# Performance work log

Hardware: AMD Instinct MI355X
Metric: run time of the kernel (lower is better)

Reference implementation:

```python
import jax, jax.numpy as jnp
import numpy as np
from jax import lax

FEAT_STRIDE = 16
N_ANCHOR = 9
PRE_NMS = 3000
POST_NMS = 300
NMS_THRESH = 0.7
MIN_SIZE = 16.0
SCALE = 1.0


def anchor_template():
    # base_size=16, ratios x scales, ratio-major flattening (matches torch loop order)
    base = 16.0
    ratios = jnp.array([0.5, 1.0, 2.0], jnp.float32)
    scales = jnp.array([8.0, 16.0, 32.0], jnp.float32)
    h = (base * scales[None, :] * jnp.sqrt(ratios)[:, None]).reshape(-1)   # [9]
    w = (base * scales[None, :] * jnp.sqrt(1.0 / ratios)[:, None]).reshape(-1)
    cy = cx = base / 2.0
    return jnp.stack([cy - h / 2, cx - w / 2, cy + h / 2, cx + w / 2], axis=1)  # [9,4] (y1,x1,y2,x2)


def shifted_anchors(hh, ww):
    base = anchor_template()
    sy = jnp.arange(hh, dtype=jnp.float32) * FEAT_STRIDE
    sx = jnp.arange(ww, dtype=jnp.float32) * FEAT_STRIDE
    sxg, syg = jnp.meshgrid(sx, sy)  # 'xy' indexing -> [hh,ww], row-major h,w ravel
    shift = jnp.stack([syg.ravel(), sxg.ravel(), syg.ravel(), sxg.ravel()], axis=1)  # [K,4]
    return (shift[:, None, :] + base[None, :, :]).reshape(-1, 4)  # [K*9,4]


def loc2bbox(anchors, loc):
    ah = anchors[:, 2] - anchors[:, 0]
    aw = anchors[:, 3] - anchors[:, 1]
    acy = anchors[:, 0] + 0.5 * ah
    acx = anchors[:, 1] + 0.5 * aw
    dy, dx, dh, dw = loc[:, 0], loc[:, 1], loc[:, 2], loc[:, 3]
    cy = dy * ah + acy
    cx = dx * aw + acx
    h = jnp.exp(dh) * ah
    w = jnp.exp(dw) * aw
    return jnp.stack([cy - 0.5 * h, cx - 0.5 * w, cy + 0.5 * h, cx + 0.5 * w], axis=1)


def pairwise_iou(b):
    area = (b[:, 2] - b[:, 0]) * (b[:, 3] - b[:, 1])  # [P]
    y1 = jnp.maximum(b[:, None, 0], b[None, :, 0])
    x1 = jnp.maximum(b[:, None, 1], b[None, :, 1])
    y2 = jnp.minimum(b[:, None, 2], b[None, :, 2])
    x2 = jnp.minimum(b[:, None, 3], b[None, :, 3])
    inter = jnp.clip(y2 - y1, 0.0) * jnp.clip(x2 - x1, 0.0)
    union = area[:, None] + area[None, :] - inter
    return jnp.where(union > 0.0, inter / union, 0.0)


def conv2d(x, W, b, pad):
    y = lax.conv_general_dilated(x, W, (1, 1), ((pad, pad), (pad, pad)),
                                 dimension_numbers=('NCHW', 'OIHW', 'NCHW'))
    return y + b[None, :, None, None]


def propose_one(loc, score, anchors, img_h, img_w):
    # loc [A,4], score [A] (fg prob)
    boxes = loc2bbox(anchors, loc)
    boxes = jnp.stack([jnp.clip(boxes[:, 0], 0.0, img_h),
                       jnp.clip(boxes[:, 1], 0.0, img_w),
                       jnp.clip(boxes[:, 2], 0.0, img_h),
                       jnp.clip(boxes[:, 3], 0.0, img_w)], axis=1)
    min_sz = MIN_SIZE * SCALE
    valid = ((boxes[:, 2] - boxes[:, 0]) >= min_sz) & ((boxes[:, 3] - boxes[:, 1]) >= min_sz)
    s = jnp.where(valid, score, -jnp.inf)
    top_s, idx = lax.top_k(s, PRE_NMS)           # sorted descending
    b = boxes[idx]                               # [PRE_NMS,4]
    iou = pairwise_iou(b)                        # [PRE_NMS,PRE_NMS]

    def body(i, keep):
        suppressed = jnp.any(keep & (iou[:, i] > NMS_THRESH))
        return keep.at[i].set(~suppressed)

    keep = lax.fori_loop(0, PRE_NMS, body, jnp.zeros(PRE_NMS, bool))
    keep = keep & jnp.isfinite(top_s)
    rank = jnp.where(keep, jnp.arange(PRE_NMS), PRE_NMS)
    order = jnp.argsort(rank)[:POST_NMS]
    roi_valid = keep[order]
    rois = jnp.where(roi_valid[:, None], b[order], 0.0)
    return rois, roi_valid


def reference(x, W1, b1, Ws, bs, Wl, bl, img_h, img_w):
    n, _, hh, ww = x.shape
    anchors = shifted_anchors(hh, ww)                       # [hh*ww*9, 4]
    h = jax.nn.relu(conv2d(x, W1, b1, 1))                   # [n,512,hh,ww]
    rpn_locs = conv2d(h, Wl, bl, 0).transpose(0, 2, 3, 1).reshape(n, -1, 4)
    rpn_scores_raw = conv2d(h, Ws, bs, 0).transpose(0, 2, 3, 1)  # [n,hh,ww,18]
    sc = rpn_scores_raw.reshape(n, hh, ww, N_ANCHOR, 2)
    fg = jax.nn.softmax(sc, axis=-1)[..., 1].reshape(n, -1)      # [n,A]
    rpn_scores = rpn_scores_raw.reshape(n, -1, 2)
    rois, roi_valid = jax.vmap(lambda l, s: propose_one(l, s, anchors, float(img_h), float(img_w)))(rpn_locs, fg)
    return rpn_locs, rpn_scores, rois, roi_valid, anchors


def setup_inputs() -> dict:
    key = jax.random.key(0)
    ks = jax.random.split(key, 4)
    n, c, hh, ww = 4, 512, 64, 64
    x = jax.random.normal(ks[0], (n, c, hh, ww), jnp.float32)
    W1 = jax.random.normal(ks[1], (512, 512, 3, 3), jnp.float32) * 0.01
    b1 = jnp.zeros((512,), jnp.float32)
    Ws = jax.random.normal(ks[2], (18, 512, 1, 1), jnp.float32) * 0.01
    bs = jnp.zeros((18,), jnp.float32)
    Wl = jax.random.normal(ks[3], (36, 512, 1, 1), jnp.float32) * 0.01
    bl = jnp.zeros((36,), jnp.float32)
    return {"x": x, "W1": W1, "b1": b1, "Ws": Ws, "bs": bs, "Wl": Wl, "bl": bl,
            "img_h": 1024, "img_w": 1024}
```

## Files before the change

kernel.cpp:

```cpp
#include <hip/hip_runtime.h>
#include <hip/hip_bf16.h>
#include <math.h>

#define N_IMG 4
#define CIN 512
#define NANCH 36864
#define PRE_NMS_N 3000
#define POST_NMS_N 300
#define NWORD 47
#define NPAIR 1128
#define PPX 4356

#define OFF_SCORES 589824
#define OFF_ROIS   884736
#define OFF_VALID  889536
#define OFF_ANCH   890736

typedef _Float16 f16x8 __attribute__((ext_vector_type(8)));
typedef float f32x4 __attribute__((ext_vector_type(4)));

__device__ __forceinline__ int swz(int p) { return (p + (p >> 2)) & 3; }

__device__ __forceinline__ unsigned long long rdlane64(unsigned long long v, int l) {
  unsigned int lo = (unsigned int)__builtin_amdgcn_readlane((int)(unsigned int)v, l);
  unsigned int hi = (unsigned int)__builtin_amdgcn_readlane((int)(unsigned int)(v >> 32), l);
  return (((unsigned long long)hi) << 32) | lo;
}

__global__ __launch_bounds__(256) void k0w_convert(
    const float* __restrict__ W1, _Float16* __restrict__ wth, _Float16* __restrict__ wtl) {
  const int tap = blockIdx.x, co0 = blockIdx.y * 32;
  for (int idx = threadIdx.x; idx < 32 * 512; idx += 256) {
    int col = idx >> 9, ci = idx & 511;
    float v = W1[(size_t)(co0 + col) * 4608 + ci * 9 + tap] * 64.0f;
    _Float16 hi = (_Float16)v;
    float lo = v - (float)hi;
    size_t o = ((size_t)(tap * 512 + co0 + col) << 9) + ci;
    wth[o] = hi; wtl[o] = (_Float16)lo;
  }
}

__global__ __launch_bounds__(256) void k0h_convert(
    const float* __restrict__ Wl, const float* __restrict__ Ws,
    _Float16* __restrict__ whdh, _Float16* __restrict__ whdl) {
  int idx = blockIdx.x * 256 + threadIdx.x;
  if (idx >= 64 * 512) return;
  int ch = idx >> 9, k = idx & 511;
  float v = 0.f;
  if (ch < 36) v = Wl[ch * 512 + k];
  else if (ch < 54) v = Ws[(ch - 36) * 512 + k];
  v *= 64.0f;
  _Float16 hi = (_Float16)v;
  float lo = v - (float)hi;
  whdh[idx] = hi; whdl[idx] = (_Float16)lo;
}

__global__ __launch_bounds__(256) void k0x_convert(
    const float* __restrict__ x, _Float16* __restrict__ xh, _Float16* __restrict__ xl,
    int img0) {
  const int bx = blockIdx.x, ci0 = blockIdx.y * 64;
  const int img_l = blockIdx.z;
  const int img = img0 + img_l;
  const size_t sbase = (size_t)img_l * PPX;
  const int tid = threadIdx.x;
  if (bx < 64) {
    __shared__ float t[64][65];
    const float* xp = x + ((size_t)img * 512 + ci0) * 4096 + bx * 64;
    for (int idx = tid; idx < 4096; idx += 256) {
      int ci_l = idx >> 6, col = idx & 63;
      t[ci_l][col] = xp[(size_t)ci_l * 4096 + col];
    }
    __syncthreads();
    for (int idx = tid; idx < 4096; idx += 256) {
      int col = idx >> 6, ci_l = idx & 63;
      float v = t[ci_l][col];
      _Float16 hi = (_Float16)v;
      float lo = v - (float)hi;
      size_t o = ((sbase + (size_t)(bx + 1) * 66 + col + 1) << 9) + ci0 + ci_l;
      xh[o] = hi; xl[o] = (_Float16)lo;
    }
  } else {
    for (int tt = tid; tt < 52 * 64; tt += 256) {
      int pl = tt >> 6, ci_l = tt & 63;
      int p = (bx - 64) * 52 + pl;
      if (p < 260) {
        int pp;
        if (p < 66) pp = p;
        else if (p < 132) pp = 65 * 66 + (p - 66);
        else if (p < 196) pp = (p - 132 + 1) * 66;
        else pp = (p - 196 + 1) * 66 + 65;
        size_t o = ((sbase + pp) << 9) + ci0 + ci_l;
        xh[o] = (_Float16)0.f; xl[o] = (_Float16)0.f;
      }
    }
  }
}

__global__ __launch_bounds__(256, 2) void k1_gemm(
    const _Float16* __restrict__ xh, const _Float16* __restrict__ xl,
    const _Float16* __restrict__ wth, const _Float16* __restrict__ wtl,
    const float* __restrict__ b1, float* __restrict__ h_out) {
  const int tid = threadIdx.x;
  const int co0 = blockIdx.x * 128;
  const int px0 = blockIdx.y * 128;
  const int img_l = px0 >> 12;
  const int y0 = (px0 & 4095) >> 6;

  __shared__ __align__(16) _Float16 AsL[4][4096];
  __shared__ __align__(16) _Float16 BsL[4][4096];

  const int lane = tid & 63, q = lane >> 4, lr = lane & 15;
  const int wid = tid >> 6, wm = wid & 1, wn = wid >> 1;

  int abase[2], bbase[2];
  #pragma unroll
  for (int it = 0; it < 2; ++it) {
    int s = it * 256 + tid;
    int pxl = s >> 2, cpos = s & 3;
    int c = cpos ^ swz(pxl);
    int row = pxl >> 6, xcol = pxl & 63;
    abase[it] = ((img_l * PPX + (y0 + row) * 66 + xcol) << 9) + c * 8;
    int bcol = s >> 2;
    int bc = (s & 3) ^ swz(bcol);
    bbase[it] = ((co0 + bcol) << 9) + bc * 8;
  }

  const int DD[9] = {0, 1, 2, 66, 67, 68, 132, 133, 134};

  f32x4 acc[4][4] = {};
  float4 rah[2], ral[2], rbh[2], rbl[2];

  #pragma unroll
  for (int it = 0; it < 2; ++it) {
    rah[it] = *(const float4*)(xh + abase[it]);
    ral[it] = *(const float4*)(xl + abase[it]);
    rbh[it] = *(const float4*)(wth + bbase[it]);
    rbl[it] = *(const float4*)(wtl + bbase[it]);
  }
  #pragma unroll
  for (int it = 0; it < 2; ++it) {
    *(float4*)&AsL[0][(it * 256 + tid) * 8] = rah[it];
    *(float4*)&AsL[1][(it * 256 + tid) * 8] = ral[it];
    *(float4*)&BsL[0][(it * 256 + tid) * 8] = rbh[it];
    *(float4*)&BsL[1][(it * 256 + tid) * 8] = rbl[it];
  }

  int tap = 0, cb = 0;
  for (int t = 0; t < 144; ++t) {
    __syncthreads();
    const int buf = t & 1;
    if (t < 143) {
      int tapn = tap + 1, cbn = cb;
      if (tapn == 9) { tapn = 0; cbn = cb + 1; }
      int ad = (DD[tapn] << 9) + cbn * 32;
      int bd = tapn * 262144 + cbn * 32;
      #pragma unroll
      for (int it = 0; it < 2; ++it) {
        rah[it] = *(const float4*)(xh + abase[it] + ad);
        ral[it] = *(const float4*)(xl + abase[it] + ad);
        rbh[it] = *(const float4*)(wth + bbase[it] + bd);
        rbl[it] = *(const float4*)(wtl + bbase[it] + bd);
      }
    }
    f16x8 ah[4], al[4], bh[4], bl[4];
    #pragma unroll
    for (int mi = 0; mi < 4; ++mi) {
      int pxl = wm * 64 + mi * 16 + lr;
      int cpr = q ^ swz(pxl);
      ah[mi] = *(const f16x8*)&AsL[buf * 2 + 0][pxl * 32 + cpr * 8];
      al[mi] = *(const f16x8*)&AsL[buf * 2 + 1][pxl * 32 + cpr * 8];
    }
    #pragma unroll
    for (int ni = 0; ni < 4; ++ni) {
      int col = wn * 64 + ni * 16 + lr;
      int cpr = q ^ swz(col);
      bh[ni] = *(const f16x8*)&BsL[buf * 2 + 0][col * 32 + cpr * 8];
      bl[ni] = *(const f16x8*)&BsL[buf * 2 + 1][col * 32 + cpr * 8];
    }
    #pragma unroll
    for (int mi = 0; mi < 4; ++mi)
      #pragma unroll
      for (int ni = 0; ni < 4; ++ni) {
        acc[mi][ni] = __builtin_amdgcn_mfma_f32_16x16x32_f16(ah[mi], bh[ni], acc[mi][ni], 0, 0, 0);
        acc[mi][ni] = __builtin_amdgcn_mfma_f32_16x16x32_f16(ah[mi], bl[ni], acc[mi][ni], 0, 0, 0);
        acc[mi][ni] = __builtin_amdgcn_mfma_f32_16x16x32_f16(al[mi], bh[ni], acc[mi][ni], 0, 0, 0);
      }
    if (t < 143) {
      int nb = (t + 1) & 1;
      #pragma unroll
      for (int it = 0; it < 2; ++it) {
        *(float4*)&AsL[nb * 2 + 0][(it * 256 + tid) * 8] = rah[it];
        *(float4*)&AsL[nb * 2 + 1][(it * 256 + tid) * 8] = ral[it];
        *(float4*)&BsL[nb * 2 + 0][(it * 256 + tid) * 8] = rbh[it];
        *(float4*)&BsL[nb * 2 + 1][(it * 256 + tid) * 8] = rbl[it];
      }
    }
    ++tap;
    if (tap == 9) { tap = 0; ++cb; }
  }

  float bb[4];
  #pragma unroll
  for (int ni = 0; ni < 4; ++ni) bb[ni] = b1[co0 + wn * 64 + ni * 16 + lr];
  #pragma unroll
  for (int mi = 0; mi < 4; ++mi)
    #pragma unroll
    for (int ni = 0; ni < 4; ++ni)
      #pragma unroll
      for (int rr = 0; rr < 4; ++rr) {
        int pxl = wm * 64 + mi * 16 + q * 4 + rr;
        int co = co0 + wn * 64 + ni * 16 + lr;
        float v = acc[mi][ni][rr] * 0.015625f + bb[ni];
        h_out[((size_t)(px0 + pxl) << 9) + co] = fmaxf(v, 0.f);
      }
}

__global__ __launch_bounds__(256, 1) void k2m_heads(
    const float* __restrict__ h,
    const _Float16* __restrict__ whdh, const _Float16* __restrict__ whdl,
    const float* __restrict__ bl, const float* __restrict__ bs,
    float* __restrict__ rpn_locs, float* __restrict__ rpn_scores,
    int img0, const int* __restrict__ ihp, const int* __restrict__ iwp,
    float* __restrict__ anchors_out, float4* __restrict__ boxes,
    unsigned long long* __restrict__ keys) {
  const int tid = threadIdx.x;
  const int px0 = blockIdx.x * 128;

  __shared__ __align__(16) _Float16 As[4][4096];
  __shared__ __align__(16) _Float16 Bs[4][2048];
  __shared__ float Cs[128][68];

  const int lane = tid & 63, q = lane >> 4, lr = lane & 15;
  const int wid = tid >> 6, wm = wid & 1, wn = wid >> 1;

  int apx[2], ac[2];
  #pragma unroll
  for (int it = 0; it < 2; ++it) {
    int s = it * 256 + tid;
    apx[it] = s >> 2;
    ac[it] = (s & 3) ^ swz(s >> 2);
  }
  const int bcol = tid >> 2, bc = (tid & 3) ^ swz(tid >> 2);

  f32x4 acc[4][2] = {};
  f16x8 rahh[2], rahl[2], rbhh, rbhl;

  #pragma unroll
  for (int it = 0; it < 2; ++it) {
    const float* src = h + ((size_t)(px0 + apx[it]) << 9) + ac[it] * 8;
    float4 v0 = *(const float4*)(src);
    float4 v1 = *(const float4*)(src + 4);
    float vv[8] = {v0.x, v0.y, v0.z, v0.w, v1.x, v1.y, v1.z, v1.w};
    f16x8 hi8, lo8;
    #pragma unroll
    for (int e = 0; e < 8; ++e) {
      _Float16 hh = (_Float16)vv[e];
      hi8[e] = hh; lo8[e] = (_Float16)(vv[e] - (float)hh);
    }
    rahh[it] = hi8; rahl[it] = lo8;
  }
  rbhh = *(const f16x8*)(whdh + bcol * 512 + bc * 8);
  rbhl = *(const f16x8*)(whdl + bcol * 512 + bc * 8);
  #pragma unroll
  for (int it = 0; it < 2; ++it) {
    *(f16x8*)&As[0][(it * 256 + tid) * 8] = rahh[it];
    *(f16x8*)&As[1][(it * 256 + tid) * 8] = rahl[it];
  }
  *(f16x8*)&Bs[0][tid * 8] = rbhh;
  *(f16x8*)&Bs[1][tid * 8] = rbhl;

  for (int t = 0; t < 16; ++t) {
    __syncthreads();
    const int buf = t & 1;
    if (t < 15) {
      const int kn = (t + 1) * 32;
      #pragma unroll
      for (int it = 0; it < 2; ++it) {
        const float* src = h + ((size_t)(px0 + apx[it]) << 9) + kn + ac[it] * 8;
        float4 v0 = *(const float4*)(src);
        float4 v1 = *(const float4*)(src + 4);
        float vv[8] = {v0.x, v0.y, v0.z, v0.w, v1.x, v1.y, v1.z, v1.w};
        f16x8 hi8, lo8;
        #pragma unroll
        for (int e = 0; e < 8; ++e) {
          _Float16 hh = (_Float16)vv[e];
          hi8[e] = hh; lo8[e] = (_Float16)(vv[e] - (float)hh);
        }
        rahh[it] = hi8; rahl[it] = lo8;
      }
      rbhh = *(const f16x8*)(whdh + bcol * 512 + kn + bc * 8);
      rbhl = *(const f16x8*)(whdl + bcol * 512 + kn + bc * 8);
    }
    f16x8 ah[4], al[4], bh[2], blo[2];
    #pragma unroll
    for (int mi = 0; mi < 4; ++mi) {
      int pxl = wm * 64 + mi * 16 + lr;
      int cpr = q ^ swz(pxl);
      ah[mi] = *(const f16x8*)&As[buf * 2 + 0][pxl * 32 + cpr * 8];
      al[mi] = *(const f16x8*)&As[buf * 2 + 1][pxl * 32 + cpr * 8];
    }
    #pragma unroll
    for (int ni = 0; ni < 2; ++ni) {
      int col = wn * 32 + ni * 16 + lr;
      int cpr = q ^ swz(col);
      bh[ni]  = *(const f16x8*)&Bs[buf * 2 + 0][col * 32 + cpr * 8];
      blo[ni] = *(const f16x8*)&Bs[buf * 2 + 1][col * 32 + cpr * 8];
    }
    #pragma unroll
    for (int mi = 0; mi < 4; ++mi)
      #pragma unroll
      for (int ni = 0; ni < 2; ++ni) {
        acc[mi][ni] = __builtin_amdgcn_mfma_f32_16x16x32_f16(ah[mi], bh[ni],  acc[mi][ni], 0, 0, 0);
        acc[mi][ni] = __builtin_amdgcn_mfma_f32_16x16x32_f16(ah[mi], blo[ni], acc[mi][ni], 0, 0, 0);
        acc[mi][ni] = __builtin_amdgcn_mfma_f32_16x16x32_f16(al[mi], bh[ni],  acc[mi][ni], 0, 0, 0);
      }
    if (t < 15) {
      int nb = (t + 1) & 1;
      #pragma unroll
      for (int it = 0; it < 2; ++it) {
        *(f16x8*)&As[nb * 2 + 0][(it * 256 + tid) * 8] = rahh[it];
        *(f16x8*)&As[nb * 2 + 1][(it * 256 + tid) * 8] = rahl[it];
      }
      *(f16x8*)&Bs[nb * 2 + 0][tid * 8] = rbhh;
      *(f16x8*)&Bs[nb * 2 + 1][tid * 8] = rbhl;
    }
  }

  #pragma unroll
  for (int mi = 0; mi < 4; ++mi)
    #pragma unroll
    for (int ni = 0; ni < 2; ++ni) {
      int ch = wn * 32 + ni * 16 + lr;
      float bias = (ch < 36) ? bl[ch] : ((ch < 54) ? bs[ch - 36] : 0.f);
      #pragma unroll
      for (int rr = 0; rr < 4; ++rr) {
        int pxl = wm * 64 + mi * 16 + q * 4 + rr;
        Cs[pxl][ch] = acc[mi][ni][rr] * 0.015625f + bias;
      }
    }
  __syncthreads();

  const float imh = (float)ihp[0], imw = (float)iwp[0];
  const float ratios[3] = {0.5f, 1.0f, 2.0f};
  const float scales[3] = {8.f, 16.f, 32.f};
  for (int t2 = tid; t2 < 128 * 9; t2 += 256) {
    int px_l = t2 / 9, a = t2 - px_l * 9;
    int pxg = px0 + px_l;
    int img = img0 + (pxg >> 12);
    int p_loc = pxg & 4095;
    size_t abase = (size_t)img * NANCH + (size_t)p_loc * 9;
    int yy = p_loc >> 6, xx = p_loc & 63;

    float4 lv; lv.x = Cs[px_l][4 * a]; lv.y = Cs[px_l][4 * a + 1];
    lv.z = Cs[px_l][4 * a + 2]; lv.w = Cs[px_l][4 * a + 3];
    *(float4*)(rpn_locs + (abase + a) * 4) = lv;
    float s0 = Cs[px_l][36 + 2 * a], s1 = Cs[px_l][36 + 2 * a + 1];
    float2 sv; sv.x = s0; sv.y = s1;
    *(float2*)(rpn_scores + (abase + a) * 2) = sv;
    float m = fmaxf(s0, s1);
    float e0 = expf(s0 - m), e1 = expf(s1 - m);
    float fgv = e1 / (e0 + e1);

    int ri = a / 3, si = a - ri * 3;
    float hh = 16.f * scales[si] * sqrtf(ratios[ri]);
    float ww = 16.f * scales[si] * sqrtf(1.0f / ratios[ri]);
    float by1 = 8.f - hh * 0.5f, bx1 = 8.f - ww * 0.5f;
    float by2 = 8.f + hh * 0.5f, bx2 = 8.f + ww * 0.5f;
    float ay1 = yy * 16.f + by1, ax1 = xx * 16.f + bx1;
    float ay2 = yy * 16.f + by2, ax2 = xx * 16.f + bx2;
    if (img == 0) {
      float* ao = anchors_out + ((size_t)p_loc * 9 + a) * 4;
      ao[0] = ay1; ao[1] = ax1; ao[2] = ay2; ao[3] = ax2;
    }
    float dy = lv.x, dx = lv.y, dh = lv.z, dw = lv.w;
    float ah2 = ay2 - ay1, aw2 = ax2 - ax1;
    float acy = ay1 + 0.5f * ah2, acx = ax1 + 0.5f * aw2;
    float cy = dy * ah2 + acy, cx = dx * aw2 + acx;
    float hb = expf(dh) * ah2, wb = expf(dw) * aw2;
    float y1 = fminf(fmaxf(cy - 0.5f * hb, 0.f), imh);
    float x1 = fminf(fmaxf(cx - 0.5f * wb, 0.f), imw);
    float y2 = fminf(fmaxf(cy + 0.5f * hb, 0.f), imh);
    float x2 = fminf(fmaxf(cx + 0.5f * wb, 0.f), imw);
    bool valid = ((y2 - y1) >= 16.0f) && ((x2 - x1) >= 16.0f);
    float s = valid ? fgv : -__builtin_inff();
    boxes[abase + a] = make_float4(y1, x1, y2, x2);
    unsigned int fb = __float_as_uint(s);
    unsigned int mono = (fb & 0x80000000u) ? ~fb : (fb | 0x80000000u);
    unsigned int ii = (unsigned int)(p_loc * 9 + a);
    keys[abase + a] = (((unsigned long long)mono) << 32) | (unsigned int)(~ii);
  }
}

__global__ __launch_bounds__(1024) void k4_select(
    const unsigned long long* __restrict__ keys, const float4* __restrict__ boxes,
    float4* __restrict__ sboxes, unsigned int* __restrict__ sfin) {
  const int n = blockIdx.x, tid = threadIdx.x;
  const int lane = tid & 63, wv = tid >> 6;
  const unsigned long long* kk = keys + (size_t)n * NANCH;
  __shared__ unsigned int hist[2048];
  __shared__ unsigned int wsum[16];
  __shared__ unsigned long long sb[4096];
  __shared__ int selb;
  __shared__ unsigned int cnt;
  unsigned long long prefix = 0ull;
  int need = PRE_NMS_N;
  const int shifts[6] = {53, 42, 31, 20, 10, 0};
  const int widths[6] = {11, 11, 11, 11, 10, 10};
  for (int rd = 0; rd < 6; ++rd) {
    const int s = shifts[rd], w = widths[rd];
    const int hib = s + w;
    for (int b = tid; b < 2048; b += 1024) hist[b] = 0u;
    __syncthreads();
    if (rd == 0) {
      for (int i = tid; i < NANCH; i += 1024) {
        unsigned long long key = kk[i];
        unsigned int bin = (unsigned int)((key >> s) & ((1u << w) - 1u));
        unsigned long long act = ~0ull;
        while (act) {
          int leader = __builtin_ctzll(act);
          unsigned int lb = (unsigned int)__shfl((int)bin, leader);
          bool same = (bin == lb);
          unsigned long long mm = __ballot(same);
          if (lane == leader) atomicAdd(&hist[lb], (unsigned int)__popcll(mm));
          act &= ~mm;
        }
      }
    } else {
      for (int i = tid; i < NANCH; i += 1024) {
        unsigned long long key = kk[i];
        bool match = ((key ^ prefix) >> hib) == 0ull;
        if (match)
          atomicAdd(&hist[(unsigned)((key >> s) & ((1u << w) - 1u))], 1u);
      }
    }
    __syncthreads();
    {
      const int base = wv * 128;
      unsigned int h0 = hist[base + 2 * lane];
      unsigned int h1 = hist[base + 2 * lane + 1];
      unsigned int x = h0 + h1;
      #pragma unroll
      for (int off2 = 1; off2 < 64; off2 <<= 1) {
        unsigned int v = __shfl_down(x, off2);
        x += (lane + off2 < 64) ? v : 0u;
      }
      if (lane == 0) wsum[wv] = x;
      __syncthreads();
      unsigned int offc = 0u;
      for (int w2 = wv + 1; w2 < 16; ++w2) offc += wsum[w2];
      hist[base + 2 * lane] = x + offc;
      hist[base + 2 * lane + 1] = x - h0 + offc;
      __syncthreads();
    }
    const int nb = 1 << w;
    for (int b = tid; b < nb; b += 1024) {
      unsigned int sv = hist[b];
      unsigned int nxt = (b + 1 < 2048) ? hist[b + 1] : 0u;
      if (sv >= (unsigned)need && nxt < (unsigned)need) selb = b;
    }
    __syncthreads();
    int bstar = selb;
    unsigned int cgt = (bstar + 1 < 2048) ? hist[bstar + 1] : 0u;
    unsigned int inbin = hist[bstar] - cgt;
    need -= (int)cgt;
    prefix |= ((unsigned long long)bstar) << s;
    __syncthreads();
    if (inbin == (unsigned)need) break;
    if ((unsigned)(PRE_NMS_N - need) + inbin <= 4096u) break;
  }
  if (tid == 0) cnt = 0u;
  __syncthreads();
  for (int i = tid; i < NANCH; i += 1024) {
    unsigned long long key = kk[i];
    if (key >= prefix) {
      unsigned int pos = atomicAdd(&cnt, 1u);
      if (pos < 4096u) sb[pos] = ~key;
    }
  }
  __syncthreads();
  unsigned int c0 = cnt;
  for (int i = tid; i < 4096; i += 1024)
    if (i >= (int)c0) sb[i] = 0xFFFFFFFFFFFFFFFFull;
  __syncthreads();
  for (int k2 = 2; k2 <= 4096; k2 <<= 1) {
    for (int j = k2 >> 1; j > 0; j >>= 1) {
      for (int t = tid; t < 2048; t += 1024) {
        int i = ((t & ~(j - 1)) << 1) | (t & (j - 1));
        int pp = i + j;
        bool up = ((i & k2) == 0);
        unsigned long long va = sb[i], vb = sb[pp];
        bool sw = up ? (va > vb) : (va < vb);
        if (sw) { sb[i] = vb; sb[pp] = va; }
      }
      __syncthreads();
    }
  }
  const float4* bx = boxes + (size_t)n * NANCH;
  for (int r = tid; r < PRE_NMS_N; r += 1024) {
    unsigned long long key = ~sb[r];
    unsigned int idx = ~((unsigned int)(key & 0xFFFFFFFFull));
    sboxes[(size_t)n * PRE_NMS_N + r] = bx[idx];
    unsigned int hi32 = (unsigned int)(key >> 32);
    sfin[n * PRE_NMS_N + r] = (hi32 > 0x007FFFFFu) ? 1u : 0u;
  }
}

__global__ __launch_bounds__(256) void k5_mask(
    const float4* __restrict__ sboxes, unsigned long long* __restrict__ mask) {
  const int n = blockIdx.y;
  const int wv = threadIdx.x >> 6, lane = threadIdx.x & 63;
  const int pid = blockIdx.x * 4 + wv;
  if (pid >= NPAIR) return;
  int c = 0, k = pid;
  while (k >= NWORD - c) { k -= NWORD - c; ++c; }
  const int wd = c + k;
  __shared__ float sA[4][64][5];
  const int j = wd * 64 + lane;
  float4 bj = sboxes[(size_t)n * PRE_NMS_N + ((j < PRE_NMS_N) ? j : 0)];
  const float aj = (bj.z - bj.x) * (bj.w - bj.y);
  const int ig = c * 64 + lane;
  float4 bi = sboxes[(size_t)n * PRE_NMS_N + ((ig < PRE_NMS_N) ? ig : 0)];
  sA[wv][lane][0] = bi.x; sA[wv][lane][1] = bi.y;
  sA[wv][lane][2] = bi.z; sA[wv][lane][3] = bi.w;
  sA[wv][lane][4] = (bi.z - bi.x) * (bi.w - bi.y);
  unsigned long long* mrow = mask + ((size_t)n * PRE_NMS_N + c * 64) * NWORD + wd;
  const int nrow = (c == NWORD - 1) ? (PRE_NMS_N - c * 64) : 64;
  for (int il = 0; il < nrow; ++il) {
    float iy1 = sA[wv][il][0], ix1 = sA[wv][il][1];
    float iy2 = sA[wv][il][2], ix2 = sA[wv][il][3], ia = sA[wv][il][4];
    float y1 = fmaxf(iy1, bj.x), x1 = fmaxf(ix1, bj.y);
    float y2 = fminf(iy2, bj.z), x2 = fminf(ix2, bj.w);
    float inter = fmaxf(y2 - y1, 0.f) * fmaxf(x2 - x1, 0.f);
    float uni = ia + aj - inter;
    float iou = (uni > 0.f) ? inter / uni : 0.f;
    bool pr = (j < PRE_NMS_N) && (iou > 0.7f);
    unsigned long long bits = __ballot(pr);
    if (lane == 0) mrow[(size_t)il * NWORD] = bits;
  }
}

__global__ __launch_bounds__(256) void k6_nms(
    const unsigned long long* __restrict__ mask, const float4* __restrict__ sboxes,
    const unsigned int* __restrict__ sfin,
    float* __restrict__ out_rois, float* __restrict__ out_valid) {
  const int n = blockIdx.x, tid = threadIdx.x;
  const int lane = tid & 63, wvq = tid >> 6;
  const unsigned long long* M = mask + (size_t)n * PRE_NMS_N * NWORD;
  __shared__ unsigned long long rows[2][64][NWORD];
  __shared__ unsigned long long keepW[NWORD];
  __shared__ unsigned long long finM[NWORD];
  __shared__ unsigned long long R[NWORD];
  __shared__ int klist[64];
  __shared__ int kcnt_sh;
  __shared__ int stopc_sh;

  if (tid == 0) stopc_sh = NWORD;
  for (int w = tid; w < NWORD; w += 256) R[w] = 0ull;

  for (int c = wvq; c < NWORD; c += 4) {
    int i = c * 64 + lane;
    int f = (i < PRE_NMS_N) ? (sfin[n * PRE_NMS_N + i] ? 1 : 0) : 0;
    unsigned long long mb = __ballot(f);
    if (lane == 0) finM[c] = mb;
  }

  #pragma unroll
  for (int j = 0; j < 12; ++j) {
    int idx = j * 256 + tid;
    if (idx < 64 * NWORD) {
      int row = idx / NWORD, w = idx - row * NWORD;
      rows[0][row][w] = M[(size_t)row * NWORD + w];
    }
  }
  __syncthreads();

  int totKF = 0;
  for (int c = 0; c < NWORD; ++c) {
    const int buf = c & 1;
    const int nIt = (c == NWORD - 1) ? (PRE_NMS_N - c * 64) : 64;
    unsigned long long pf[12];
    const bool hasNext = (c + 1 < NWORD);
    if (hasNext) {
      const int i1 = (c + 1) * 64;
      #pragma unroll
      for (int j = 0; j < 12; ++j) {
        int idx = j * 256 + tid;
        if (idx < 64 * NWORD) {
          int row = idx / NWORD, w = idx - row * NWORD;
          int gi = i1 + row;
          pf[j] = (gi < PRE_NMS_N) ? M[(size_t)gi * NWORD + w] : 0ull;
        }
      }
    }
    if (tid < 64) {
      unsigned long long Dcur = rows[buf][lane][c];
      unsigned long long rem = R[c];
      unsigned long long und = ~rem;
      if (nIt < 64) und &= ((1ull << nIt) - 1ull);
      unsigned long long kept = 0ull;
      while (und) {
        int b = __builtin_ctzll(und);
        kept |= (1ull << b);
        unsigned long long db = rdlane64(Dcur, b);
        und &= ~db;
        und &= ~(1ull << b);
      }
      totKF += (int)__popcll(kept & finM[c]);
      if (lane == 0) {
        keepW[c] = kept; kcnt_sh = (int)__popcll(kept);
        if (totKF >= POST_NMS_N && stopc_sh == NWORD) stopc_sh = c;
      }
      if ((kept >> lane) & 1ull) {
        int r = (int)__popcll(kept & ((1ull << lane) - 1ull));
        klist[r] = lane;
      }
    }
    __syncthreads();
    if (stopc_sh <= c) break;
    {
      const int kc = kcnt_sh;
      const int w0 = c + 1;
      const int nw = NWORD - w0;
      const int tot = kc * nw;
      for (int it2 = tid; it2 < tot; it2 += 256) {
        int ki = it2 / nw, w = w0 + (it2 - ki * nw);
        int b = klist[ki];
        unsigned long long v = rows[buf][b][w];
        if (v) atomicOr(&R[w], v);
      }
    }
    if (hasNext) {
      #pragma unroll
      for (int j = 0; j < 12; ++j) {
        int idx = j * 256 + tid;
        if (idx < 64 * NWORD) {
          int row = idx / NWORD, w = idx - row * NWORD;
          rows[buf ^ 1][row][w] = pf[j];
        }
      }
    }
    __syncthreads();
  }

  if (tid < 64) {
    const int cstop = stopc_sh;
    const unsigned int* fin = sfin + n * PRE_NMS_N;
    int running = 0;
    for (int c = 0; c < NWORD && c <= cstop; ++c) {
      int i = c * 64 + lane;
      unsigned long long kw = keepW[c];
      int kf = 0;
      if (i < PRE_NMS_N) kf = (int)((kw >> lane) & 1ull) & (fin[i] ? 1 : 0);
      unsigned long long m = __ballot(kf);
      if (kf) {
        int r = running + __popcll(m & ((1ull << lane) - 1ull));
        if (r < POST_NMS_N) {
          float4 b4 = sboxes[(size_t)n * PRE_NMS_N + i];
          float* o = out_rois + (size_t)(n * POST_NMS_N + r) * 4;
          o[0] = b4.x; o[1] = b4.y; o[2] = b4.z; o[3] = b4.w;
          out_valid[n * POST_NMS_N + r] = 1.0f;
        }
      }
      running += __popcll(m);
    }
    int keptTotal = running;
    if (keptTotal < POST_NMS_N) {
      int runN = 0;
      for (int c = 0; c < NWORD && keptTotal + runN < POST_NMS_N; ++c) {
        int i = c * 64 + lane;
        unsigned long long kw = keepW[c];
        int nf = 0;
        if (i < PRE_NMS_N) nf = !(((kw >> lane) & 1ull) && fin[i]);
        unsigned long long m = __ballot(nf);
        if (nf) {
          int r = keptTotal + runN + __popcll(m & ((1ull << lane) - 1ull));
          if (r < POST_NMS_N) {
            float* o = out_rois + (size_t)(n * POST_NMS_N + r) * 4;
            o[0] = 0.f; o[1] = 0.f; o[2] = 0.f; o[3] = 0.f;
            out_valid[n * POST_NMS_N + r] = 0.0f;
          }
        }
        runN += __popcll(m);
      }
    }
  }
}

extern "C" void kernel_launch(void* const* d_in, const int* in_sizes, int n_in,
                              void* d_out, int out_size, void* d_ws, size_t ws_size,
                              hipStream_t stream) {
  const float* x  = (const float*)d_in[0];
  const float* W1 = (const float*)d_in[1];
  const float* b1 = (const float*)d_in[2];
  const float* Ws = (const float*)d_in[3];
  const float* bs = (const float*)d_in[4];
  const float* Wl = (const float*)d_in[5];
  const float* bl = (const float*)d_in[6];
  const int* ihp  = (const int*)d_in[7];
  const int* iwp  = (const int*)d_in[8];

  float* out = (float*)d_out;
  float* o_locs   = out;
  float* o_scores = out + OFF_SCORES;
  float* o_rois   = out + OFF_ROIS;
  float* o_valid  = out + OFF_VALID;
  float* o_anch   = out + OFF_ANCH;

  char* ws = (char*)d_ws;
  const size_t OFF_WTH = 0;
  const size_t OFF_WTL = 4718592;
  const size_t OFF_WHD = 9437184;
  const size_t OFF_DYN = 11796480;

  const size_t PER_IMG = 4460544ull * 2 + 8388608ull;
  int nipp;
  if (ws_size >= OFF_DYN + 4 * PER_IMG) nipp = 4;
  else if (ws_size >= OFF_DYN + 2 * PER_IMG) nipp = 2;
  else nipp = 1;
  const int nph = N_IMG / nipp;

  _Float16* wth  = (_Float16*)(ws + OFF_WTH);
  _Float16* wtl  = (_Float16*)(ws + OFF_WTL);
  _Float16* whdh = (_Float16*)(ws + OFF_WHD);
  _Float16* whdl = (_Float16*)(ws + OFF_WHD + 65536);
  _Float16* xh   = (_Float16*)(ws + OFF_DYN);
  _Float16* xl   = (_Float16*)(ws + OFF_DYN + (size_t)nipp * 4460544);
  float* h       = (float*)(ws + OFF_DYN + (size_t)nipp * 8921088);

  float4* boxes            = (float4*)(ws + OFF_DYN);
  unsigned long long* keys = (unsigned long long*)(ws + OFF_DYN + 2359296);
  float4* sboxes           = (float4*)(ws + OFF_DYN + 3538944);
  unsigned int* sfin       = (unsigned int*)(ws + OFF_DYN + 3730944);
  unsigned long long* mask = (unsigned long long*)(ws + OFF_DYN + 3778944);

  if (nph > 1) {
    size_t tail = OFF_DYN + (size_t)nipp * PER_IMG;
    boxes  = (float4*)(ws + tail);
    keys   = (unsigned long long*)(ws + tail + 2359296);
    sboxes = (float4*)(ws + tail + 3538944);
    sfin   = (unsigned int*)(ws + tail + 3730944);
    mask   = (unsigned long long*)(ws + tail + 3778944);
  }

  k0w_convert<<<dim3(9, 16), 256, 0, stream>>>(W1, wth, wtl);
  k0h_convert<<<128, 256, 0, stream>>>(Wl, Ws, whdh, whdl);

  for (int ph = 0; ph < nph; ++ph) {
    int img0 = ph * nipp;
    k0x_convert<<<dim3(69, 8, nipp), 256, 0, stream>>>(x, xh, xl, img0);
    k1_gemm<<<dim3(4, nipp * 32), 256, 0, stream>>>(xh, xl, wth, wtl, b1, h);
    k2m_heads<<<dim3(nipp * 32), 256, 0, stream>>>(h, whdh, whdl, bl, bs,
                                                   o_locs, o_scores, img0,
                                                   ihp, iwp, o_anch, boxes, keys);
  }

  k4_select<<<4, 1024, 0, stream>>>(keys, boxes, sboxes, sfin);
  k5_mask<<<dim3((NPAIR + 3) / 4, 4), 256, 0, stream>>>(sboxes, mask);
  k6_nms<<<4, 256, 0, stream>>>(mask, sboxes, sfin, o_rois, o_valid);
}
```

Before: 507.2 us.

## Rewrite NMS as single-wave kernel with async LDS loads; merge weight conversions

The NMS kernel now runs one 64-lane wave per image instead of 256 threads. The removed-mask accumulator lives in registers, read with readlane, so the block barriers and shared atomics go away. Mask rows are prefetched straight into LDS with global_load_lds, double-buffered, and the fin bits are balloted inline. The two weight-conversion kernels are merged into one launch to save launch overhead. The risk is that the serial per-wave update loop and the lower parallelism on the mask loads could lengthen the critical path.

```diff
diff --git a/kernel.cpp b/kernel.cpp
--- a/kernel.cpp
+++ b/kernel.cpp
@@ -27,32 +27,40 @@
   return (((unsigned long long)hi) << 32) | lo;
 }
 
-__global__ __launch_bounds__(256) void k0w_convert(
-    const float* __restrict__ W1, _Float16* __restrict__ wth, _Float16* __restrict__ wtl) {
-  const int tap = blockIdx.x, co0 = blockIdx.y * 32;
-  for (int idx = threadIdx.x; idx < 32 * 512; idx += 256) {
-    int col = idx >> 9, ci = idx & 511;
-    float v = W1[(size_t)(co0 + col) * 4608 + ci * 9 + tap] * 64.0f;
-    _Float16 hi = (_Float16)v;
-    float lo = v - (float)hi;
-    size_t o = ((size_t)(tap * 512 + co0 + col) << 9) + ci;
-    wth[o] = hi; wtl[o] = (_Float16)lo;
-  }
-}
-
-__global__ __launch_bounds__(256) void k0h_convert(
+__device__ __forceinline__ void gl_lds16(const void* g, void* l) {
+  __builtin_amdgcn_global_load_lds(
+      (const __attribute__((address_space(1))) unsigned int*)g,
+      (__attribute__((address_space(3))) unsigned int*)l, 16, 0, 0);
+}
+
+__global__ __launch_bounds__(256) void k0wh_convert(
+    const float* __restrict__ W1, _Float16* __restrict__ wth, _Float16* __restrict__ wtl,
     const float* __restrict__ Wl, const float* __restrict__ Ws,
     _Float16* __restrict__ whdh, _Float16* __restrict__ whdl) {
-  int idx = blockIdx.x * 256 + threadIdx.x;
-  if (idx >= 64 * 512) return;
-  int ch = idx >> 9, k = idx & 511;
-  float v = 0.f;
-  if (ch < 36) v = Wl[ch * 512 + k];
-  else if (ch < 54) v = Ws[(ch - 36) * 512 + k];
-  v *= 64.0f;
-  _Float16 hi = (_Float16)v;
-  float lo = v - (float)hi;
-  whdh[idx] = hi; whdl[idx] = (_Float16)lo;
+  const int bx = blockIdx.x;
+  if (bx < 144) {
+    const int tap = bx % 9, co0 = (bx / 9) * 32;
+    for (int idx = threadIdx.x; idx < 32 * 512; idx += 256) {
+      int col = idx >> 9, ci = idx & 511;
+      float v = W1[(size_t)(co0 + col) * 4608 + ci * 9 + tap] * 64.0f;
+      _Float16 hi = (_Float16)v;
+      float lo = v - (float)hi;
+      size_t o = ((size_t)(tap * 512 + co0 + col) << 9) + ci;
+      wth[o] = hi; wtl[o] = (_Float16)lo;
+    }
+  } else {
+    int idx = (bx - 144) * 256 + threadIdx.x;
+    if (idx < 64 * 512) {
+      int ch = idx >> 9, k = idx & 511;
+      float v = 0.f;
+      if (ch < 36) v = Wl[ch * 512 + k];
+      else if (ch < 54) v = Ws[(ch - 36) * 512 + k];
+      v *= 64.0f;
+      _Float16 hi = (_Float16)v;
+      float lo = v - (float)hi;
+      whdh[idx] = hi; whdl[idx] = (_Float16)lo;
+    }
+  }
 }
 
 __global__ __launch_bounds__(256) void k0x_convert(
@@ -539,111 +547,85 @@
   }
 }
 
-__global__ __launch_bounds__(256) void k6_nms(
+__global__ __launch_bounds__(64) void k6_nms(
     const unsigned long long* __restrict__ mask, const float4* __restrict__ sboxes,
     const unsigned int* __restrict__ sfin,
     float* __restrict__ out_rois, float* __restrict__ out_valid) {
-  const int n = blockIdx.x, tid = threadIdx.x;
-  const int lane = tid & 63, wvq = tid >> 6;
+  const int n = blockIdx.x, lane = threadIdx.x;
   const unsigned long long* M = mask + (size_t)n * PRE_NMS_N * NWORD;
-  __shared__ unsigned long long rows[2][64][NWORD];
+  __shared__ __align__(16) unsigned long long rows[2][64][NWORD];
   __shared__ unsigned long long keepW[NWORD];
-  __shared__ unsigned long long finM[NWORD];
-  __shared__ unsigned long long R[NWORD];
-  __shared__ int klist[64];
-  __shared__ int kcnt_sh;
-  __shared__ int stopc_sh;
-
-  if (tid == 0) stopc_sh = NWORD;
-  for (int w = tid; w < NWORD; w += 256) R[w] = 0ull;
-
-  for (int c = wvq; c < NWORD; c += 4) {
-    int i = c * 64 + lane;
-    int f = (i < PRE_NMS_N) ? (sfin[n * PRE_NMS_N + i] ? 1 : 0) : 0;
-    unsigned long long mb = __ballot(f);
-    if (lane == 0) finM[c] = mb;
-  }
-
-  #pragma unroll
-  for (int j = 0; j < 12; ++j) {
-    int idx = j * 256 + tid;
-    if (idx < 64 * NWORD) {
-      int row = idx / NWORD, w = idx - row * NWORD;
-      rows[0][row][w] = M[(size_t)row * NWORD + w];
-    }
-  }
-  __syncthreads();
-
+
+  {
+    const char* src = (const char*)M;
+    char* dst = (char*)&rows[0][0][0];
+    for (int u = 0; u < 24; ++u) {
+      int idx = u * 64 + lane;
+      if (idx < 1504) gl_lds16(src + idx * 16, dst + idx * 16);
+    }
+  }
+  asm volatile("s_waitcnt vmcnt(0)" ::: "memory");
+  __builtin_amdgcn_sched_barrier(0);
+
+  unsigned long long Rw = 0ull;
   int totKF = 0;
+  int stopc = NWORD;
+  int buf = 0;
   for (int c = 0; c < NWORD; ++c) {
-    const int buf = c & 1;
     const int nIt = (c == NWORD - 1) ? (PRE_NMS_N - c * 64) : 64;
-    unsigned long long pf[12];
     const bool hasNext = (c + 1 < NWORD);
     if (hasNext) {
       const int i1 = (c + 1) * 64;
-      #pragma unroll
-      for (int j = 0; j < 12; ++j) {
-        int idx = j * 256 + tid;
-        if (idx < 64 * NWORD) {
-          int row = idx / NWORD, w = idx - row * NWORD;
-          int gi = i1 + row;
-          pf[j] = (gi < PRE_NMS_N) ? M[(size_t)gi * NWORD + w] : 0ull;
-        }
-      }
-    }
-    if (tid < 64) {
-      unsigned long long Dcur = rows[buf][lane][c];
-      unsigned long long rem = R[c];
-      unsigned long long und = ~rem;
-      if (nIt < 64) und &= ((1ull << nIt) - 1ull);
-      unsigned long long kept = 0ull;
-      while (und) {
-        int b = __builtin_ctzll(und);
-        kept |= (1ull << b);
-        unsigned long long db = rdlane64(Dcur, b);
-        und &= ~db;
-        und &= ~(1ull << b);
-      }
-      totKF += (int)__popcll(kept & finM[c]);
-      if (lane == 0) {
-        keepW[c] = kept; kcnt_sh = (int)__popcll(kept);
-        if (totKF >= POST_NMS_N && stopc_sh == NWORD) stopc_sh = c;
-      }
-      if ((kept >> lane) & 1ull) {
-        int r = (int)__popcll(kept & ((1ull << lane) - 1ull));
-        klist[r] = lane;
-      }
-    }
-    __syncthreads();
-    if (stopc_sh <= c) break;
+      const int nrows = (i1 + 64 <= PRE_NMS_N) ? 64 : (PRE_NMS_N - i1);
+      const int units = (nrows * NWORD) >> 1;
+      const char* src = (const char*)(M + (size_t)i1 * NWORD);
+      char* dst = (char*)&rows[buf ^ 1][0][0];
+      for (int u = 0; u < 24; ++u) {
+        int idx = u * 64 + lane;
+        if (idx < units) gl_lds16(src + idx * 16, dst + idx * 16);
+      }
+    }
+    unsigned long long Dcur = rows[buf][lane][c];
+    unsigned long long rem = rdlane64(Rw, c);
+    unsigned long long und = ~rem;
+    if (nIt < 64) und &= ((1ull << nIt) - 1ull);
+    unsigned long long kept = 0ull;
+    while (und) {
+      int b = __builtin_ctzll(und);
+      kept |= (1ull << b);
+      unsigned long long db = rdlane64(Dcur, b);
+      und &= ~db;
+      und &= ~(1ull << b);
+    }
     {
-      const int kc = kcnt_sh;
-      const int w0 = c + 1;
-      const int nw = NWORD - w0;
-      const int tot = kc * nw;
-      for (int it2 = tid; it2 < tot; it2 += 256) {
-        int ki = it2 / nw, w = w0 + (it2 - ki * nw);
-        int b = klist[ki];
-        unsigned long long v = rows[buf][b][w];
-        if (v) atomicOr(&R[w], v);
+      int i = c * 64 + lane;
+      int f = (i < PRE_NMS_N) ? (sfin[n * PRE_NMS_N + i] ? 1 : 0) : 0;
+      unsigned long long fM = __ballot(f);
+      totKF += (int)__popcll(kept & fM);
+    }
+    if (lane == 0) keepW[c] = kept;
+    if (totKF >= POST_NMS_N && stopc == NWORD) stopc = c;
+    if (stopc <= c) break;
+    {
+      unsigned long long kk2 = kept;
+      const bool upd = (lane > c) && (lane < NWORD);
+      while (kk2) {
+        int b = __builtin_ctzll(kk2); kk2 &= kk2 - 1ull;
+        unsigned long long v = rows[buf][b][lane];
+        if (upd) Rw |= v;
       }
     }
     if (hasNext) {
-      #pragma unroll
-      for (int j = 0; j < 12; ++j) {
-        int idx = j * 256 + tid;
-        if (idx < 64 * NWORD) {
-          int row = idx / NWORD, w = idx - row * NWORD;
-          rows[buf ^ 1][row][w] = pf[j];
-        }
-      }
-    }
-    __syncthreads();
-  }
-
-  if (tid < 64) {
-    const int cstop = stopc_sh;
+      asm volatile("s_waitcnt vmcnt(0)" ::: "memory");
+      __builtin_amdgcn_sched_barrier(0);
+    }
+    buf ^= 1;
+  }
+  asm volatile("s_waitcnt vmcnt(0)" ::: "memory");
+  __syncthreads();
+
+  {
+    const int cstop = stopc;
     const unsigned int* fin = sfin + n * PRE_NMS_N;
     int running = 0;
     for (int c = 0; c < NWORD && c <= cstop; ++c) {
@@ -742,8 +724,7 @@
     mask   = (unsigned long long*)(ws + tail + 3778944);
   }
 
-  k0w_convert<<<dim3(9, 16), 256, 0, stream>>>(W1, wth, wtl);
-  k0h_convert<<<128, 256, 0, stream>>>(Wl, Ws, whdh, whdl);
+  k0wh_convert<<<272, 256, 0, stream>>>(W1, wth, wtl, Wl, Ws, whdh, whdl);
 
   for (int ph = 0; ph < nph; ++ph) {
     int img0 = ph * nipp;
@@ -756,5 +737,5 @@
 
   k4_select<<<4, 1024, 0, stream>>>(keys, boxes, sboxes, sfin);
   k5_mask<<<dim3((NPAIR + 3) / 4, 4), 256, 0, stream>>>(sboxes, mask);
-  k6_nms<<<4, 256, 0, stream>>>(mask, sboxes, sfin, o_rois, o_valid);
-}
+  k6_nms<<<4, 64, 0, stream>>>(mask, sboxes, sfin, o_rois, o_valid);
+}
```

New measurement: 520.1 us. +2.5%, slower.
